# Optimization experiments

Measured on AMD Instinct MI355X. Metric: run time of the kernel, lower is better.

Reference implementation:

```python
import jax, jax.numpy as jnp
import numpy as np

T = 5       # fixed temporal factor in the original forward
HEADS = 8
DIM = 512
DIM_HEAD = 64
INNER = HEADS * DIM_HEAD  # 512 (must equal DIM for the masked scatter)


def setup_inputs() -> dict:
    key = jax.random.key(0)
    ks = jax.random.split(key, 8)
    bt, n = 40, 3137  # b=8, t=5; n-1 = 56*56 visual tokens
    x = jax.random.normal(ks[0], (bt, n, DIM), dtype=jnp.float32)
    mask = jax.random.randint(ks[1], (bt, 56, 56), 0, 2).astype(jnp.float32)
    s = 1.0 / np.sqrt(DIM)
    w_vq = jax.random.normal(ks[2], (DIM, INNER), dtype=jnp.float32) * s
    w_vkv = jax.random.normal(ks[3], (DIM, 2 * INNER), dtype=jnp.float32) * s
    w_aqkv = jax.random.normal(ks[4], (DIM, 3 * INNER), dtype=jnp.float32) * s
    w_out = jax.random.normal(ks[5], (INNER, DIM), dtype=jnp.float32) * s
    b_out = jnp.zeros((DIM,), dtype=jnp.float32)
    return {"x": x, "mask": mask, "w_vq": w_vq, "w_vkv": w_vkv,
            "w_aqkv": w_aqkv, "w_out": w_out, "b_out": b_out}


def reference(x, mask, w_vq, w_vkv, w_aqkv, w_out, b_out):
    bt, n, dim = x.shape
    b = bt // T
    nv = n - 1
    dh = DIM_HEAD
    scale = dh ** -0.5

    A = x[:, 0]        # (bt, dim) -- single 'action' token per frame
    V = x[:, 1:]       # (bt, nv, dim)
    m = mask.reshape(bt, nv, 1)

    aq, ak, av = jnp.split(A @ w_aqkv, 3, axis=-1)      # each (bt, INNER)
    vk, vv = jnp.split(V @ w_vkv, 2, axis=-1)           # each (bt, nv, INNER)
    vq = V @ w_vq                                        # (bt, nv, INNER)

    # --- A -> V cross attention: per batch, T A-queries over T*nv V keys ---
    qa = aq.reshape(b, T, HEADS, dh)
    Kv = vk.reshape(b, T * nv, HEADS, dh)
    Vv = vv.reshape(b, T * nv, HEADS, dh)
    av_dots = jnp.einsum('bqhd,bkhd->bhqk', qa, Kv) * scale
    av_attn = jax.nn.softmax(av_dots, axis=-1)
    av_o = jnp.einsum('bhqk,bkhd->bqhd', av_attn, Vv)   # (b, T, H, dh)
    a_out = av_o.reshape(bt, 1, INNER)

    # --- V -> A cross attention with block mask: every V token attends only
    # to its own batch's T A-tokens (the -inf block fill in the original) ---
    Qv = vq.reshape(b, T, nv, HEADS, dh)
    Ka = ak.reshape(b, T, HEADS, dh)
    Va = av.reshape(b, T, HEADS, dh)
    va_dots = jnp.einsum('bfnhd,bkhd->bhfnk', Qv, Ka) * scale
    va_attn = jax.nn.softmax(va_dots, axis=-1)          # softmax over T keys
    va_o = jnp.einsum('bhfnk,bkhd->bfnhd', va_attn, Va)
    v_full = va_o.reshape(bt, nv, INNER)

    # original: scatter attn out into V.clone() then * mask, under no_grad()
    # => masked positions get attention output, others V*0 = 0; detached.
    v_out = jax.lax.stop_gradient(v_full * m)

    out = jnp.concatenate([a_out, v_out], axis=1)       # (bt, n, INNER)
    return out @ w_out + b_out
```

## Files before the change

### kernel.cpp

```cpp
#include <hip/hip_runtime.h>

typedef unsigned short u16;
typedef unsigned int u32;
typedef __attribute__((ext_vector_type(8))) u16 u16x8;
typedef __attribute__((ext_vector_type(8))) __bf16 bf16x8;
typedef __attribute__((ext_vector_type(4))) float f32x4;

__device__ __forceinline__ float b2f(u16 u){ return __uint_as_float(((u32)u)<<16); }
__device__ __forceinline__ u16 f2b(float f){
  u32 b = __float_as_uint(f);
  return (u16)((b + 0x7fffu + ((b>>16)&1u))>>16);
}
__device__ __forceinline__ void gload16(const void* g, void* l){
  __builtin_amdgcn_global_load_lds((__attribute__((address_space(1))) void*)g,
                                   (__attribute__((address_space(3))) void*)l, 16, 0, 0);
}
__device__ __forceinline__ float wred_max(float v){
#pragma unroll
  for (int o=32;o>0;o>>=1) v = fmaxf(v, __shfl_xor(v,o));
  return v;
}
__device__ __forceinline__ float wred_sum(float v){
#pragma unroll
  for (int o=32;o>0;o>>=1) v += __shfl_xor(v,o);
  return v;
}


__global__ void k_pre(const float* __restrict__ x, const float* __restrict__ wvq,
                      const float* __restrict__ wvkv, const float* __restrict__ wout,
                      const float* __restrict__ waqkv,
                      u16* __restrict__ xb, u16* __restrict__ W1T,
                      u16* __restrict__ WoutT, float* __restrict__ aqkv){
  const int bid = blockIdx.x, tid = threadIdx.x;
  if (bid < 2048){
    const int stride = 2048*256;
    for (int i = bid*256 + tid; i < 8030720; i += stride){
      const float4* p = (const float4*)(x + (size_t)i*8);
      float4 a = p[0], b = p[1];
      u16x8 o;
      o[0]=f2b(a.x); o[1]=f2b(a.y); o[2]=f2b(a.z); o[3]=f2b(a.w);
      o[4]=f2b(b.x); o[5]=f2b(b.y); o[6]=f2b(b.z); o[7]=f2b(b.w);
      *(u16x8*)(xb + (size_t)i*8) = o;
    }
  } else if (bid < 6144){
    int id = (bid-2048)*256 + tid;
    if (id < 786432){
      int n = id >> 9, k = id & 511;
      float v;
      if (n < 512){
        v = wvq[k*512 + n];
      } else {
        int j = n - 512, h = j >> 7, r = j & 127;
        int c2 = (r < 64) ? (h*64 + r) : (512 + h*64 + (r - 64));
        v = wvkv[k*1024 + c2];
      }
      W1T[id] = f2b(v);
    } else {
      int j = id - 786432;
      int n = j >> 9, k = j & 511;
      WoutT[j] = f2b(wout[k*512 + n]);
    }
  } else {
    int id = (bid-6144)*256 + tid;
    int bt = id / 1536, c = id % 1536;
    const float* xr = x + (size_t)bt*3137*512;
    float s = 0.f;
    for (int k=0;k<512;k++) s += xr[k]*waqkv[k*1536+c];
    aqkv[id] = s;
  }
}

template<int FOUT>
__global__ __launch_bounds__(512, 2) void k_gemm256(
    const u16* __restrict__ A, const u16* __restrict__ BT,
    int M, int N, int K, int NX,
    u16* __restrict__ Cb, float* __restrict__ Cf, const float* __restrict__ bias)
{
  __shared__ __align__(16) char Ls[4][32768];
  const int tid = threadIdx.x;
  const int wid = tid >> 6, lane = tid & 63;
  const int nwg = gridDim.x, orig = blockIdx.x;
  const int q8 = nwg >> 3, r8 = nwg & 7;
  const int xc = orig & 7, sl = orig >> 3;
  const int work = (xc < r8 ? xc*(q8+1) : r8*(q8+1) + (xc-r8)*q8) + sl;
  const int m0 = (work / NX) * 256, n0 = (work % NX) * 256;
  const size_t K2 = (size_t)K * 2;
  const char* Ab = (const char*)A;
  const char* Bb = (const char*)BT;
  size_t asrc[2], bsrc[2];
  const int ad0 = wid*1024, ad1 = 8192 + wid*1024;
#pragma unroll
  for (int i=0;i<2;i++){
    int row = (i*8 + wid)*16 + (lane & 15);
    int koff = (lane >> 4) << 4;
    int ra = m0 + row; if (ra >= M) ra = M - 1;
    asrc[i] = (size_t)ra * K2 + koff;
    bsrc[i] = (size_t)(n0 + row) * K2 + koff;
  }
#define STAGE(s4, ks) { \
    size_t ko = (size_t)(ks) * 64; \
    gload16(Ab + asrc[0] + ko, Ls[s4] + ad0); \
    gload16(Ab + asrc[1] + ko, Ls[s4] + ad1); \
    gload16(Bb + bsrc[0] + ko, Ls[s4] + 16384 + ad0); \
    gload16(Bb + bsrc[1] + ko, Ls[s4] + 16384 + ad1); }

  f32x4 acc[8][4] = {};
  const int awb = (wid >> 2) * 8192;
  const int bwb = 16384 + (wid & 3) * 4096;
  const int NS = K >> 5;
  STAGE(0,0) STAGE(1,1) STAGE(2,2)
  for (int s = 0; s < NS; ++s){
    if (s + 2 < NS)      { asm volatile("s_waitcnt vmcnt(8)" ::: "memory"); }
    else if (s + 1 < NS) { asm volatile("s_waitcnt vmcnt(4)" ::: "memory"); }
    else                 { asm volatile("s_waitcnt vmcnt(0)" ::: "memory"); }
    __builtin_amdgcn_s_barrier();
    __builtin_amdgcn_sched_barrier(0);
    if (s + 3 < NS) STAGE((s+3)&3, s+3)
    const char* base = Ls[s & 3];
    bf16x8 af[8], bfr[4];
#pragma unroll
    for (int i=0;i<4;i++) af[i]  = *(const bf16x8*)(base + awb + i*1024 + lane*16);
#pragma unroll
    for (int i=0;i<4;i++) bfr[i] = *(const bf16x8*)(base + bwb + i*1024 + lane*16);
    asm volatile("s_waitcnt lgkmcnt(0)" ::: "memory");
    __builtin_amdgcn_sched_barrier(0);
    __builtin_amdgcn_s_setprio(1);
#pragma unroll
    for (int mr=0;mr<4;mr++)
#pragma unroll
      for (int nc=0;nc<4;nc++)
        acc[mr][nc] = __builtin_amdgcn_mfma_f32_16x16x32_bf16(af[mr], bfr[nc], acc[mr][nc], 0,0,0);
    __builtin_amdgcn_s_setprio(0);
#pragma unroll
    for (int i=4;i<8;i++) af[i] = *(const bf16x8*)(base + awb + i*1024 + lane*16);
    asm volatile("s_waitcnt lgkmcnt(0)" ::: "memory");
    __builtin_amdgcn_sched_barrier(0);
    __builtin_amdgcn_s_setprio(1);
#pragma unroll
    for (int mr=4;mr<8;mr++)
#pragma unroll
      for (int nc=0;nc<4;nc++)
        acc[mr][nc] = __builtin_amdgcn_mfma_f32_16x16x32_bf16(af[mr], bfr[nc], acc[mr][nc], 0,0,0);
    __builtin_amdgcn_s_setprio(0);
  }
#undef STAGE
  const int wm = (wid >> 2) * 128, wn = (wid & 3) * 64;
  if (m0 + 256 <= M){
#pragma unroll
    for (int mr=0;mr<8;mr++){
#pragma unroll
      for (int nc=0;nc<4;nc++){
#pragma unroll
        for (int rg=0;rg<4;rg++){
          int row = m0 + wm + mr*16 + ((lane>>4)<<2) + rg;
          int col = n0 + wn + nc*16 + (lane&15);
          float v = acc[mr][nc][rg];
          if (FOUT) Cf[(size_t)row*N + col] = v + bias[col];
          else      Cb[(size_t)row*N + col] = f2b(v);
        }
      }
    }
  } else {
#pragma unroll
    for (int mr=0;mr<8;mr++){
#pragma unroll
      for (int nc=0;nc<4;nc++){
#pragma unroll
        for (int rg=0;rg<4;rg++){
          int row = m0 + wm + mr*16 + ((lane>>4)<<2) + rg;
          int col = n0 + wn + nc*16 + (lane&15);
          if (row < M){
            float v = acc[mr][nc][rg];
            if (FOUT) Cf[(size_t)row*N + col] = v + bias[col];
            else      Cb[(size_t)row*N + col] = f2b(v);
          }
        }
      }
    }
  }
}

__global__ __launch_bounds__(320) void k_attn(
    const u16* __restrict__ out1, const float* __restrict__ aqkv,
    const float* __restrict__ mask,
    float* __restrict__ pm, float* __restrict__ pl, float* __restrict__ pacc,
    u16* __restrict__ IN)
{
  __shared__ __align__(16) char smem[32768];
  const int bid = blockIdx.x, tid = threadIdx.x;
  if (bid < 1024){
    char* Ksm = smem;
    char* Vsm = smem + 16384;
    const int sp = bid & 15, bh = bid >> 4, b = bh >> 3, h = bh & 7;
    const int wid = tid >> 6, lane = tid & 63;
    const int q = wid;
    float qreg[64];
    {
      const float* ap = aqkv + ((size_t)(b*5+q)*1536 + h*64);
#pragma unroll
      for (int d=0; d<64; d++) qreg[d] = ap[d];
    }
    float m = -1e30f, l = 0.f;
    float acc[8] = {0,0,0,0,0,0,0,0};
    const int g0 = sp * 980;
    for (int c = 0; c < 8; c++){
      for (int idx = tid; idx < 2048; idx += 320){
        int r = idx >> 4, g = idx & 15;
        int loc = c*128 + r; if (loc > 979) loc = 979;
        int gk = g0 + loc;
        int tk = gk / 3136, nv = gk - tk*3136;
        size_t grow = (size_t)((b*5+tk)*3137 + 1 + nv)*1536 + 512 + h*128 + g*8;
        u16x8 v = *(const u16x8*)(out1 + grow);
        char* dst = (g < 8) ? Ksm : Vsm;
        int seg = g & 7;
        *(u16x8*)(dst + r*128 + ((seg*16) ^ ((r&7)<<4))) = v;
      }
      __syncthreads();
      float s0 = 0.f, s1 = 0.f;
#pragma unroll
      for (int seg=0; seg<8; seg++){
        const int r0 = lane, r1 = 64 + lane;
        u16x8 k0 = *(const u16x8*)(Ksm + r0*128 + ((seg*16) ^ ((r0&7)<<4)));
        u16x8 k1 = *(const u16x8*)(Ksm + r1*128 + ((seg*16) ^ ((r1&7)<<4)));
#pragma unroll
        for (int j=0;j<8;j++){
          s0 += qreg[seg*8+j]*b2f(k0[j]);
          s1 += qreg[seg*8+j]*b2f(k1[j]);
        }
      }
      s0 *= 0.125f; s1 *= 0.125f;
      const int locbase = c*128;
      if (locbase + lane >= 980)      s0 = -1e30f;
      if (locbase + 64 + lane >= 980) s1 = -1e30f;
      float cmax = wred_max(fmaxf(s0, s1));
      float mn = fmaxf(m, cmax);
      float resc = __expf(m - mn);
      float p0 = (s0 > -1e29f) ? __expf(s0 - mn) : 0.f;
      float p1 = (s1 > -1e29f) ? __expf(s1 - mn) : 0.f;
      l = l*resc + wred_sum(p0 + p1);
#pragma unroll
      for (int j=0;j<8;j++) acc[j] *= resc;
      const int g = lane >> 3, cc = lane & 7;
#pragma unroll
      for (int i=0;i<16;i++){
        int k = i*8 + g;
        u16x8 vv = *(const u16x8*)(Vsm + k*128 + ((cc*16) ^ ((k&7)<<4)));
        float p = (i < 8) ? __shfl(p0, k) : __shfl(p1, k-64);
#pragma unroll
        for (int j=0;j<8;j++) acc[j] += p*b2f(vv[j]);
      }
      m = mn;
      __syncthreads();
    }
#pragma unroll
    for (int j=0;j<8;j++){
      float v = acc[j];
      v += __shfl_xor(v, 8); v += __shfl_xor(v, 16); v += __shfl_xor(v, 32);
      acc[j] = v;
    }
    const int base = (bh*16 + sp)*5 + q;
    if (lane == 0){ pm[base] = m; pl[base] = l; }
    if (lane < 8){
      float* pa = pacc + (size_t)base*64 + lane*8;
#pragma unroll
      for (int j=0;j<8;j++) pa[j] = acc[j];
    }
  } else {
    float (*Ka)[8][68] = (float(*)[8][68])smem;
    float (*Va)[8][68] = (float(*)[8][68])(smem + 10880);
    const int fid = bid - 1024;
    const int b = fid / 392, bx = fid % 392;
    for (int i = tid; i < 2560; i += 320){
      int t = i >> 9, rem = i & 511, hh = rem >> 6, d = rem & 63;
      const float* src = aqkv + (size_t)(b*5+t)*1536;
      Ka[t][hh][d] = src[512 + hh*64 + d];
      Va[t][hh][d] = src[1024 + hh*64 + d];
    }
    __syncthreads();
    const int task = bx*320 + tid;
    const int h = task & 7, rl = task >> 3;
    const int f = rl / 3136, nv = rl - f*3136;
    const int bt = b*5 + f;
    const size_t r1 = (size_t)bt*3137 + 1 + nv;
    u16* op = IN + r1*512 + h*64;
    const float mraw = mask[(size_t)bt*3136 + nv];
    if (mraw == 0.f){
      u16x8 z = {};
#pragma unroll
      for (int sg=0; sg<8; sg++) *(u16x8*)(op + sg*8) = z;
    } else {
      const u16* qp = out1 + r1*1536 + h*64;
      float qf[64];
#pragma unroll
      for (int sg=0; sg<8; sg++){
        u16x8 v = *(const u16x8*)(qp + sg*8);
#pragma unroll
        for (int j=0;j<8;j++) qf[sg*8+j] = b2f(v[j]);
      }
      float sd[5];
#pragma unroll
      for (int t=0;t<5;t++){
        float s = 0.f;
#pragma unroll
        for (int d=0;d<64;d++) s += qf[d]*Ka[t][h][d];
        sd[t] = s*0.125f;
      }
      float mx = sd[0];
#pragma unroll
      for (int t=1;t<5;t++) mx = fmaxf(mx, sd[t]);
      float p[5], ps = 0.f;
#pragma unroll
      for (int t=0;t<5;t++){ p[t] = __expf(sd[t]-mx); ps += p[t]; }
      const float mv = mraw / ps;
#pragma unroll
      for (int sg=0; sg<8; sg++){
        u16x8 o;
#pragma unroll
        for (int j=0;j<8;j++){
          const int d = sg*8+j;
          float v = 0.f;
#pragma unroll
          for (int t=0;t<5;t++) v += p[t]*Va[t][h][d];
          o[j] = f2b(v*mv);
        }
        *(u16x8*)(op + sg*8) = o;
      }
    }
  }
}

__global__ void k_combine(const float* __restrict__ pm, const float* __restrict__ pl,
                          const float* __restrict__ pacc, u16* __restrict__ IN)
{
  const int id = blockIdx.x;
  const int q = id % 5, t2 = id / 5;
  const int h = t2 & 7, b = t2 >> 3;
  const int d = threadIdx.x;
  const int bh = b*8 + h;
  float ms = -1e30f;
#pragma unroll
  for (int s2=0;s2<16;s2++) ms = fmaxf(ms, pm[(bh*16+s2)*5+q]);
  float L = 0.f, o = 0.f;
#pragma unroll
  for (int s2=0;s2<16;s2++){
    int base = (bh*16+s2)*5+q;
    float w = __expf(pm[base]-ms);
    L += w*pl[base];
    o += w*pacc[(size_t)base*64 + d];
  }
  IN[(size_t)(b*5+q)*3137*512 + h*64 + d] = f2b(o / L);
}

extern "C" void kernel_launch(void* const* d_in, const int* in_sizes, int n_in,
                              void* d_out, int out_size, void* d_ws, size_t ws_size,
                              hipStream_t stream)
{
  const float* x      = (const float*)d_in[0];
  const float* mask   = (const float*)d_in[1];
  const float* w_vq   = (const float*)d_in[2];
  const float* w_vkv  = (const float*)d_in[3];
  const float* w_aqkv = (const float*)d_in[4];
  const float* w_out  = (const float*)d_in[5];
  const float* b_out  = (const float*)d_in[6];
  float* out = (float*)d_out;
  char* ws = (char*)d_ws;

  constexpr size_t MR = 125480;
  constexpr size_t OFF_XB   = 0;
  constexpr size_t OFF_OUT1 = OFF_XB + MR*512*2;
  constexpr size_t OFF_W1T  = OFF_OUT1 + MR*1536*2;
  constexpr size_t OFF_WOT  = OFF_W1T + 1536*512*2;
  constexpr size_t OFF_AQKV = OFF_WOT + 512*512*2;
  constexpr size_t OFF_PM   = OFF_AQKV + 40*1536*4;
  constexpr size_t OFF_PL   = OFF_PM + 5120*4;
  constexpr size_t OFF_PACC = OFF_PL + 5120*4;

  u16* Xb     = (u16*)(ws + OFF_XB);
  u16* out1   = (u16*)(ws + OFF_OUT1);
  u16* W1T    = (u16*)(ws + OFF_W1T);
  u16* WoutT  = (u16*)(ws + OFF_WOT);
  float* aqkv = (float*)(ws + OFF_AQKV);
  float* pm   = (float*)(ws + OFF_PM);
  float* pl   = (float*)(ws + OFF_PL);
  float* pacc = (float*)(ws + OFF_PACC);

  k_pre<<<6384, 256, 0, stream>>>(x, w_vq, w_vkv, w_out, w_aqkv, Xb, W1T, WoutT, aqkv);
  k_gemm256<0><<<2946, 512, 0, stream>>>(Xb, W1T, (int)MR, 1536, 512, 6,
                                         out1, nullptr, nullptr);
  k_attn<<<4160, 320, 0, stream>>>(out1, aqkv, mask, pm, pl, pacc, Xb);
  k_combine<<<320, 64, 0, stream>>>(pm, pl, pacc, Xb);
  k_gemm256<1><<<982, 512, 0, stream>>>(Xb, WoutT, (int)MR, 512, 512, 2,
                                        nullptr, out, b_out);
}
```

Baseline: 785.0 us.

## Shrink GEMM tile to 256x128 with triple-buffered LDS for higher occupancy

The GEMM kernel moves from 256x256 tiles with a 4-stage LDS ring to 256x128 tiles with a 3-stage ring. Each wave now computes a 64x64 sub-tile instead of 128x64, and the launch bounds request 4 workgroups per CU instead of 2. Grid sizes double to cover the narrower tiles. The aim is more resident waves to hide latency and better balance of tiles across CUs, at the cost of lower operand reuse per tile and a shallower prefetch pipeline.

```diff
diff --git a/kernel.cpp b/kernel.cpp
--- a/kernel.cpp
+++ b/kernel.cpp
@@ -72,53 +72,58 @@
 }
 
 template<int FOUT>
-__global__ __launch_bounds__(512, 2) void k_gemm256(
+__global__ __launch_bounds__(512, 4) void k_gemm(
     const u16* __restrict__ A, const u16* __restrict__ BT,
     int M, int N, int K, int NX,
     u16* __restrict__ Cb, float* __restrict__ Cf, const float* __restrict__ bias)
 {
-  __shared__ __align__(16) char Ls[4][32768];
+  __shared__ __align__(16) char Ls[3][24576];
   const int tid = threadIdx.x;
   const int wid = tid >> 6, lane = tid & 63;
   const int nwg = gridDim.x, orig = blockIdx.x;
   const int q8 = nwg >> 3, r8 = nwg & 7;
   const int xc = orig & 7, sl = orig >> 3;
   const int work = (xc < r8 ? xc*(q8+1) : r8*(q8+1) + (xc-r8)*q8) + sl;
-  const int m0 = (work / NX) * 256, n0 = (work % NX) * 256;
+  const int m0 = (work / NX) * 256, n0 = (work % NX) * 128;
   const size_t K2 = (size_t)K * 2;
   const char* Ab = (const char*)A;
   const char* Bb = (const char*)BT;
-  size_t asrc[2], bsrc[2];
+  size_t asrc[2], bsrc;
   const int ad0 = wid*1024, ad1 = 8192 + wid*1024;
-#pragma unroll
-  for (int i=0;i<2;i++){
-    int row = (i*8 + wid)*16 + (lane & 15);
-    int koff = (lane >> 4) << 4;
-    int ra = m0 + row; if (ra >= M) ra = M - 1;
-    asrc[i] = (size_t)ra * K2 + koff;
-    bsrc[i] = (size_t)(n0 + row) * K2 + koff;
-  }
-#define STAGE(s4, ks) { \
+  const int bd  = 16384 + wid*1024;
+  {
+    const int koff = (lane >> 4) << 4;
+#pragma unroll
+    for (int i=0;i<2;i++){
+      int ra = m0 + (i*8 + wid)*16 + (lane & 15);
+      if (ra >= M) ra = M - 1;
+      asrc[i] = (size_t)ra * K2 + koff;
+    }
+    bsrc = (size_t)(n0 + wid*16 + (lane & 15)) * K2 + koff;
+  }
+#define STAGE(s3, ks) { \
     size_t ko = (size_t)(ks) * 64; \
-    gload16(Ab + asrc[0] + ko, Ls[s4] + ad0); \
-    gload16(Ab + asrc[1] + ko, Ls[s4] + ad1); \
-    gload16(Bb + bsrc[0] + ko, Ls[s4] + 16384 + ad0); \
-    gload16(Bb + bsrc[1] + ko, Ls[s4] + 16384 + ad1); }
-
-  f32x4 acc[8][4] = {};
-  const int awb = (wid >> 2) * 8192;
-  const int bwb = 16384 + (wid & 3) * 4096;
+    gload16(Ab + asrc[0] + ko, Ls[s3] + ad0); \
+    gload16(Ab + asrc[1] + ko, Ls[s3] + ad1); \
+    gload16(Bb + bsrc + ko, Ls[s3] + bd); }
+
+  f32x4 acc[4][4] = {};
+  const int awb = (wid >> 1) * 4096;
+  const int bwb = 16384 + (wid & 1) * 4096;
   const int NS = K >> 5;
-  STAGE(0,0) STAGE(1,1) STAGE(2,2)
+  STAGE(0,0) STAGE(1,1)
+  int cur = 0;
   for (int s = 0; s < NS; ++s){
-    if (s + 2 < NS)      { asm volatile("s_waitcnt vmcnt(8)" ::: "memory"); }
-    else if (s + 1 < NS) { asm volatile("s_waitcnt vmcnt(4)" ::: "memory"); }
-    else                 { asm volatile("s_waitcnt vmcnt(0)" ::: "memory"); }
+    if (s + 1 < NS) { asm volatile("s_waitcnt vmcnt(3)" ::: "memory"); }
+    else            { asm volatile("s_waitcnt vmcnt(0)" ::: "memory"); }
     __builtin_amdgcn_s_barrier();
     __builtin_amdgcn_sched_barrier(0);
-    if (s + 3 < NS) STAGE((s+3)&3, s+3)
-    const char* base = Ls[s & 3];
-    bf16x8 af[8], bfr[4];
+    if (s + 2 < NS){
+      int sp = cur + 2; if (sp >= 3) sp -= 3;
+      STAGE(sp, s+2)
+    }
+    const char* base = Ls[cur];
+    bf16x8 af[4], bfr[4];
 #pragma unroll
     for (int i=0;i<4;i++) af[i]  = *(const bf16x8*)(base + awb + i*1024 + lane*16);
 #pragma unroll
@@ -132,23 +137,13 @@
       for (int nc=0;nc<4;nc++)
         acc[mr][nc] = __builtin_amdgcn_mfma_f32_16x16x32_bf16(af[mr], bfr[nc], acc[mr][nc], 0,0,0);
     __builtin_amdgcn_s_setprio(0);
-#pragma unroll
-    for (int i=4;i<8;i++) af[i] = *(const bf16x8*)(base + awb + i*1024 + lane*16);
-    asm volatile("s_waitcnt lgkmcnt(0)" ::: "memory");
-    __builtin_amdgcn_sched_barrier(0);
-    __builtin_amdgcn_s_setprio(1);
-#pragma unroll
-    for (int mr=4;mr<8;mr++)
-#pragma unroll
-      for (int nc=0;nc<4;nc++)
-        acc[mr][nc] = __builtin_amdgcn_mfma_f32_16x16x32_bf16(af[mr], bfr[nc], acc[mr][nc], 0,0,0);
-    __builtin_amdgcn_s_setprio(0);
+    cur = (cur + 1 == 3) ? 0 : cur + 1;
   }
 #undef STAGE
-  const int wm = (wid >> 2) * 128, wn = (wid & 3) * 64;
+  const int wm = (wid >> 1) * 64, wn = (wid & 1) * 64;
   if (m0 + 256 <= M){
 #pragma unroll
-    for (int mr=0;mr<8;mr++){
+    for (int mr=0;mr<4;mr++){
 #pragma unroll
       for (int nc=0;nc<4;nc++){
 #pragma unroll
@@ -163,7 +158,7 @@
     }
   } else {
 #pragma unroll
-    for (int mr=0;mr<8;mr++){
+    for (int mr=0;mr<4;mr++){
 #pragma unroll
       for (int nc=0;nc<4;nc++){
 #pragma unroll
@@ -386,10 +381,10 @@
   float* pacc = (float*)(ws + OFF_PACC);
 
   k_pre<<<6384, 256, 0, stream>>>(x, w_vq, w_vkv, w_out, w_aqkv, Xb, W1T, WoutT, aqkv);
-  k_gemm256<0><<<2946, 512, 0, stream>>>(Xb, W1T, (int)MR, 1536, 512, 6,
-                                         out1, nullptr, nullptr);
+  k_gemm<0><<<5892, 512, 0, stream>>>(Xb, W1T, (int)MR, 1536, 512, 12,
+                                      out1, nullptr, nullptr);
   k_attn<<<4160, 320, 0, stream>>>(out1, aqkv, mask, pm, pl, pacc, Xb);
   k_combine<<<320, 64, 0, stream>>>(pm, pl, pacc, Xb);
-  k_gemm256<1><<<982, 512, 0, stream>>>(Xb, WoutT, (int)MR, 512, 512, 2,
-                                        nullptr, out, b_out);
-}
+  k_gemm<1><<<1964, 512, 0, stream>>>(Xb, WoutT, (int)MR, 512, 512, 4,
+                                      nullptr, out, b_out);
+}
```

New measurement: 859.9 us. 9.5% more time.
